# Optimization experiments

Hardware: AMD Instinct MI355X
Metric: run time of the kernel (lower is better)

The kernel has to match this reference:

```python
import jax, jax.numpy as jnp
import numpy as np

N = 50000
E = 800000
IN_DIM = 128
HIDDEN = 256
HEADS = 8
HEAD_DIM = HIDDEN // HEADS  # 32
NUM_CLASSES = 40
NEG_SLOPE = 0.2


def setup_inputs() -> dict:
    key = jax.random.key(0)
    ks = jax.random.split(key, 16)
    x = jax.random.normal(ks[0], (N, IN_DIM), dtype=jnp.float32)
    edge_index = jax.random.randint(ks[1], (2, E), 0, N, dtype=jnp.int64)

    def glorot(k, shape, fan_in):
        return jax.random.normal(k, shape, dtype=jnp.float32) / np.sqrt(fan_in)

    # layer 1: in -> heads*head_dim (concat)
    W1 = glorot(ks[2], (IN_DIM, HEADS * HEAD_DIM), IN_DIM)
    as1 = glorot(ks[3], (HEADS, HEAD_DIM), HEAD_DIM)
    ad1 = glorot(ks[4], (HEADS, HEAD_DIM), HEAD_DIM)
    b1 = jnp.zeros((HEADS * HEAD_DIM,), dtype=jnp.float32)
    # layer 2: hidden -> heads*head_dim (concat)
    W2 = glorot(ks[5], (HIDDEN, HEADS * HEAD_DIM), HIDDEN)
    as2 = glorot(ks[6], (HEADS, HEAD_DIM), HEAD_DIM)
    ad2 = glorot(ks[7], (HEADS, HEAD_DIM), HEAD_DIM)
    b2 = jnp.zeros((HEADS * HEAD_DIM,), dtype=jnp.float32)
    # layer 3: hidden -> num_classes, 1 head, no concat (mean == identity for 1 head)
    W3 = glorot(ks[8], (HIDDEN, 1 * NUM_CLASSES), HIDDEN)
    as3 = glorot(ks[9], (1, NUM_CLASSES), NUM_CLASSES)
    ad3 = glorot(ks[10], (1, NUM_CLASSES), NUM_CLASSES)
    b3 = jnp.zeros((NUM_CLASSES,), dtype=jnp.float32)
    return {"x": x, "edge_index": edge_index,
            "W1": W1, "as1": as1, "ad1": ad1, "b1": b1,
            "W2": W2, "as2": as2, "ad2": ad2, "b2": b2,
            "W3": W3, "as3": as3, "ad3": ad3, "b3": b3}


def _segment_softmax(logits, seg, n):
    # logits: [E, H]; softmax per destination node
    m = jax.ops.segment_max(logits, seg, num_segments=n)
    m = jnp.where(jnp.isfinite(m), m, 0.0)  # empty segments -> 0
    e = jnp.exp(logits - m[seg])
    s = jax.ops.segment_sum(e, seg, num_segments=n)
    return e / (s[seg] + 1e-16)


def _gat_layer(x, src, dst, W, a_src, a_dst, b, heads, concat):
    n = x.shape[0]
    h = (x @ W).reshape(n, heads, -1)                    # [N, H, D]
    al_s = jnp.einsum('nhd,hd->nh', h, a_src)            # [N, H]
    al_d = jnp.einsum('nhd,hd->nh', h, a_dst)            # [N, H]
    e = jax.nn.leaky_relu(al_s[src] + al_d[dst], NEG_SLOPE)  # [E, H]
    alpha = _segment_softmax(e, dst, n)                  # [E, H]
    msg = h[src] * alpha[..., None]                      # [E, H, D]
    out = jax.ops.segment_sum(msg, dst, num_segments=n)  # [N, H, D]
    out = out.reshape(n, -1) if concat else out.mean(axis=1)
    return out + b


def reference(x, edge_index, W1, as1, ad1, b1, W2, as2, ad2, b2, W3, as3, ad3, b3):
    # add self loops (PyG GATConv default)
    loops = jnp.arange(N, dtype=edge_index.dtype)
    src = jnp.concatenate([edge_index[0], loops])
    dst = jnp.concatenate([edge_index[1], loops])
    # eval mode: dropout is a no-op
    h = _gat_layer(x, src, dst, W1, as1, ad1, b1, HEADS, True)
    h = jax.nn.elu(h)
    h = _gat_layer(h, src, dst, W2, as2, ad2, b2, HEADS, True)
    h = jax.nn.elu(h)
    out = _gat_layer(h, src, dst, W3, as3, ad3, b3, 1, False)
    return out
```

## Files before the change

kernel.cpp:

```cpp
#include <hip/hip_runtime.h>
#include <hip/hip_bf16.h>

#define NEG_SLOPE 0.2f

typedef __attribute__((ext_vector_type(8))) short bf16x8;
typedef __attribute__((ext_vector_type(4))) float f32x4;

__device__ __forceinline__ unsigned short f2bf(float v) {
    union { float f; unsigned int u; } x; x.f = v;
    unsigned int r = x.u + 0x7fffu + ((x.u >> 16) & 1u);
    return (unsigned short)(r >> 16);
}
__device__ __forceinline__ float bf2f(unsigned short b) {
    union { unsigned int u; float f; } x; x.u = ((unsigned int)b) << 16;
    return x.f;
}


__global__ void count_edges_k(const int* __restrict__ ei, int E, int n, int* __restrict__ cnt) {
    int e = blockIdx.x * 256 + threadIdx.x;
    int ET = E + n;
    if (e >= ET) return;
    int d = (e < E) ? ei[E + e] : (e - E);
    atomicAdd(&cnt[d], 1);
}

__global__ void scan1_k(const int* __restrict__ cnt, int* __restrict__ row_ptr,
                        int* __restrict__ bsums, int n) {
    __shared__ int sd[256];
    int b = blockIdx.x, t = threadIdx.x;
    int base = b * 1024 + t * 4;
    int v[4];
    int loc = 0;
#pragma unroll
    for (int j = 0; j < 4; ++j) {
        v[j] = (base + j < n) ? cnt[base + j] : 0;
        loc += v[j];
    }
    sd[t] = loc;
    __syncthreads();
    for (int off = 1; off < 256; off <<= 1) {
        int x = (t >= off) ? sd[t - off] : 0;
        __syncthreads();
        sd[t] += x;
        __syncthreads();
    }
    int run = sd[t] - loc;
    if (t == 255) bsums[b] = sd[t];
#pragma unroll
    for (int j = 0; j < 4; ++j) {
        if (base + j < n) row_ptr[base + j] = run;
        run += v[j];
    }
}

__global__ void scan2_k(int* __restrict__ bsums, int nb) {
    if (threadIdx.x == 0 && blockIdx.x == 0) {
        int run = 0;
        for (int i = 0; i < nb; ++i) { int x = bsums[i]; bsums[i] = run; run += x; }
    }
}

__global__ void scan3_k(int* __restrict__ row_ptr, int* __restrict__ pos,
                        const int* __restrict__ bsums, int n, int total) {
    int idx = blockIdx.x * 256 + threadIdx.x;
    if (idx < n) {
        int vv = row_ptr[idx] + bsums[idx >> 10];
        row_ptr[idx] = vv;
        pos[idx] = vv;
    } else if (idx == n) {
        row_ptr[n] = total;
    }
}

__global__ void scatter_edges_k(const int* __restrict__ ei, int E, int n,
                                int* __restrict__ pos, int* __restrict__ srcs) {
    int e = blockIdx.x * 256 + threadIdx.x;
    int ET = E + n;
    if (e >= ET) return;
    int s, d;
    if (e < E) { s = ei[e]; d = ei[E + e]; }
    else       { s = e - E; d = e - E; }
    int idx = atomicAdd(&pos[d], 1);
    srcs[idx] = s;
}


__global__ void convert_w_k(const float* __restrict__ W,
                            unsigned short* __restrict__ Bh, unsigned short* __restrict__ Bl,
                            int K, int Nc) {
    int idx = blockIdx.x * 256 + threadIdx.x;
    if (idx >= K * Nc) return;
    int k = idx / Nc, c = idx - k * Nc;
    float v = W[idx];
    unsigned short h = f2bf(v);
    float r = v - bf2f(h);
    Bh[c * K + k] = h;
    Bl[c * K + k] = f2bf(r);
}


#define GPAD 40

__global__ __launch_bounds__(256) void mfma_gemm_k(const float* __restrict__ A,
                                                   const unsigned short* __restrict__ Bh,
                                                   const unsigned short* __restrict__ Bl,
                                                   unsigned short* __restrict__ Cb,
                                                   int M, int K, int Nc) {
    __shared__ unsigned short Ash[128][GPAD];
    __shared__ unsigned short Asl[128][GPAD];
    __shared__ unsigned short Bsh[128][GPAD];
    __shared__ unsigned short Bsl[128][GPAD];

    int bm = blockIdx.y * 128;
    int bn = blockIdx.x * 128;
    int t = threadIdx.x;
    int w = t >> 6, l = t & 63;
    int wm = w >> 1, wn = w & 1;
    int lr = l & 15, lk = (l >> 4) * 8;

    int srow = t >> 1;
    int skh  = (t & 1) * 16;

    f32x4 acc[4][4];
#pragma unroll
    for (int i = 0; i < 4; ++i)
#pragma unroll
        for (int j = 0; j < 4; ++j)
            acc[i][j] = (f32x4){0.f, 0.f, 0.f, 0.f};

    const int arow = bm + srow;
    const bool arow_ok = (arow < M);
    const size_t acol_base = (size_t)arow * K + skh;
    const size_t bcol_base = (size_t)(bn + srow) * K + skh;

    for (int k0 = 0; k0 < K; k0 += 32) {
        float vv[16];
        if (arow_ok) {
            const float4* ap = reinterpret_cast<const float4*>(A + acol_base + k0);
#pragma unroll
            for (int q = 0; q < 4; ++q) {
                float4 v4 = ap[q];
                vv[4 * q + 0] = v4.x; vv[4 * q + 1] = v4.y;
                vv[4 * q + 2] = v4.z; vv[4 * q + 3] = v4.w;
            }
        } else {
#pragma unroll
            for (int q = 0; q < 16; ++q) vv[q] = 0.f;
        }
        unsigned int hw[8], lw[8];
#pragma unroll
        for (int q = 0; q < 8; ++q) {
            unsigned short h0 = f2bf(vv[2 * q]);
            unsigned short h1 = f2bf(vv[2 * q + 1]);
            unsigned short l0 = f2bf(vv[2 * q] - bf2f(h0));
            unsigned short l1 = f2bf(vv[2 * q + 1] - bf2f(h1));
            hw[q] = (unsigned int)h0 | ((unsigned int)h1 << 16);
            lw[q] = (unsigned int)l0 | ((unsigned int)l1 << 16);
        }
        __syncthreads();
        {
            uint4* dh = reinterpret_cast<uint4*>(&Ash[srow][skh]);
            uint4* dl = reinterpret_cast<uint4*>(&Asl[srow][skh]);
            dh[0] = make_uint4(hw[0], hw[1], hw[2], hw[3]);
            dh[1] = make_uint4(hw[4], hw[5], hw[6], hw[7]);
            dl[0] = make_uint4(lw[0], lw[1], lw[2], lw[3]);
            dl[1] = make_uint4(lw[4], lw[5], lw[6], lw[7]);
        }
        {
            const uint4* sh = reinterpret_cast<const uint4*>(Bh + bcol_base + k0);
            const uint4* sl = reinterpret_cast<const uint4*>(Bl + bcol_base + k0);
            uint4* dh = reinterpret_cast<uint4*>(&Bsh[srow][skh]);
            uint4* dl = reinterpret_cast<uint4*>(&Bsl[srow][skh]);
            dh[0] = sh[0]; dh[1] = sh[1];
            dl[0] = sl[0]; dl[1] = sl[1];
        }
        __syncthreads();

        bf16x8 ah[4], al[4], bh[4], bl[4];
#pragma unroll
        for (int i = 0; i < 4; ++i) {
            int r = wm * 64 + i * 16 + lr;
            ah[i] = *reinterpret_cast<const bf16x8*>(&Ash[r][lk]);
            al[i] = *reinterpret_cast<const bf16x8*>(&Asl[r][lk]);
        }
#pragma unroll
        for (int j = 0; j < 4; ++j) {
            int c = wn * 64 + j * 16 + lr;
            bh[j] = *reinterpret_cast<const bf16x8*>(&Bsh[c][lk]);
            bl[j] = *reinterpret_cast<const bf16x8*>(&Bsl[c][lk]);
        }
#pragma unroll
        for (int i = 0; i < 4; ++i)
#pragma unroll
            for (int j = 0; j < 4; ++j) {
                acc[i][j] = __builtin_amdgcn_mfma_f32_16x16x32_bf16(ah[i], bh[j], acc[i][j], 0, 0, 0);
                acc[i][j] = __builtin_amdgcn_mfma_f32_16x16x32_bf16(ah[i], bl[j], acc[i][j], 0, 0, 0);
                acc[i][j] = __builtin_amdgcn_mfma_f32_16x16x32_bf16(al[i], bh[j], acc[i][j], 0, 0, 0);
            }
    }

#pragma unroll
    for (int i = 0; i < 4; ++i) {
#pragma unroll
        for (int r = 0; r < 4; ++r) {
            int row_g = bm + wm * 64 + i * 16 + (l >> 4) * 4 + r;
            if (row_g >= M) continue;
#pragma unroll
            for (int j = 0; j < 4; ++j) {
                int col_g = bn + wn * 64 + j * 16 + lr;
                Cb[(size_t)row_g * Nc + col_g] = f2bf(acc[i][j][r]);
            }
        }
    }
}


__global__ __launch_bounds__(256) void gemm_bf16a_k(const unsigned short* __restrict__ A,
                                                    const unsigned short* __restrict__ Bh,
                                                    const unsigned short* __restrict__ Bl,
                                                    unsigned short* __restrict__ Cb,
                                                    int M, int K, int Nc) {
    __shared__ unsigned short As[128][GPAD];
    __shared__ unsigned short Bsh[128][GPAD];
    __shared__ unsigned short Bsl[128][GPAD];

    int bm = blockIdx.y * 128;
    int bn = blockIdx.x * 128;
    int t = threadIdx.x;
    int w = t >> 6, l = t & 63;
    int wm = w >> 1, wn = w & 1;
    int lr = l & 15, lk = (l >> 4) * 8;

    int srow = t >> 1;
    int skh  = (t & 1) * 16;

    f32x4 acc[4][4];
#pragma unroll
    for (int i = 0; i < 4; ++i)
#pragma unroll
        for (int j = 0; j < 4; ++j)
            acc[i][j] = (f32x4){0.f, 0.f, 0.f, 0.f};

    const int arow = bm + srow;
    const bool arow_ok = (arow < M);
    const size_t acol_base = (size_t)arow * K + skh;
    const size_t bcol_base = (size_t)(bn + srow) * K + skh;

    for (int k0 = 0; k0 < K; k0 += 32) {
        __syncthreads();
        {
            uint4* da = reinterpret_cast<uint4*>(&As[srow][skh]);
            if (arow_ok) {
                const uint4* sa = reinterpret_cast<const uint4*>(A + acol_base + k0);
                da[0] = sa[0]; da[1] = sa[1];
            } else {
                da[0] = make_uint4(0u, 0u, 0u, 0u);
                da[1] = make_uint4(0u, 0u, 0u, 0u);
            }
            const uint4* sh = reinterpret_cast<const uint4*>(Bh + bcol_base + k0);
            const uint4* sl = reinterpret_cast<const uint4*>(Bl + bcol_base + k0);
            uint4* dh = reinterpret_cast<uint4*>(&Bsh[srow][skh]);
            uint4* dl = reinterpret_cast<uint4*>(&Bsl[srow][skh]);
            dh[0] = sh[0]; dh[1] = sh[1];
            dl[0] = sl[0]; dl[1] = sl[1];
        }
        __syncthreads();

        bf16x8 ah[4], bh[4], bl[4];
#pragma unroll
        for (int i = 0; i < 4; ++i) {
            int r = wm * 64 + i * 16 + lr;
            ah[i] = *reinterpret_cast<const bf16x8*>(&As[r][lk]);
        }
#pragma unroll
        for (int j = 0; j < 4; ++j) {
            int c = wn * 64 + j * 16 + lr;
            bh[j] = *reinterpret_cast<const bf16x8*>(&Bsh[c][lk]);
            bl[j] = *reinterpret_cast<const bf16x8*>(&Bsl[c][lk]);
        }
#pragma unroll
        for (int i = 0; i < 4; ++i)
#pragma unroll
            for (int j = 0; j < 4; ++j) {
                acc[i][j] = __builtin_amdgcn_mfma_f32_16x16x32_bf16(ah[i], bh[j], acc[i][j], 0, 0, 0);
                acc[i][j] = __builtin_amdgcn_mfma_f32_16x16x32_bf16(ah[i], bl[j], acc[i][j], 0, 0, 0);
            }
    }

#pragma unroll
    for (int i = 0; i < 4; ++i) {
#pragma unroll
        for (int r = 0; r < 4; ++r) {
            int row_g = bm + wm * 64 + i * 16 + (l >> 4) * 4 + r;
            if (row_g >= M) continue;
#pragma unroll
            for (int j = 0; j < 4; ++j) {
                int col_g = bn + wn * 64 + j * 16 + lr;
                Cb[(size_t)row_g * Nc + col_g] = f2bf(acc[i][j][r]);
            }
        }
    }
}


__global__ __launch_bounds__(256) void compute_al_k(const unsigned short* __restrict__ h,
                                                    const float* __restrict__ a_src,
                                                    const float* __restrict__ a_dst,
                                                    float* __restrict__ al_s,
                                                    float* __restrict__ al_d, int n) {
    int wid = threadIdx.x >> 6, lane = threadIdx.x & 63;
    int node = blockIdx.x * 4 + wid;
    if (node >= n) return;
    ushort4 v = reinterpret_cast<const ushort4*>(h + (size_t)node * 256)[lane];
    float4 asv = reinterpret_cast<const float4*>(a_src)[lane];
    float4 adv = reinterpret_cast<const float4*>(a_dst)[lane];
    float ps = bf2f(v.x) * asv.x + bf2f(v.y) * asv.y + bf2f(v.z) * asv.z + bf2f(v.w) * asv.w;
    float pd = bf2f(v.x) * adv.x + bf2f(v.y) * adv.y + bf2f(v.z) * adv.z + bf2f(v.w) * adv.w;
#pragma unroll
    for (int off = 1; off < 8; off <<= 1) {
        ps += __shfl_xor(ps, off, 64);
        pd += __shfl_xor(pd, off, 64);
    }
    if ((lane & 7) == 0) {
        al_s[node * 8 + (lane >> 3)] = ps;
        al_d[node * 8 + (lane >> 3)] = pd;
    }
}

__global__ void compute_al3_k(const unsigned short* __restrict__ h,
                              const float* __restrict__ a_src, const float* __restrict__ a_dst,
                              float* __restrict__ al_s, float* __restrict__ al_d, int n) {
    int wid = threadIdx.x >> 6, lane = threadIdx.x & 63;
    int node = blockIdx.x * 4 + wid;
    if (node >= n) return;
    float hv = (lane < 40) ? bf2f(h[(size_t)node * 128 + lane]) : 0.f;
    float ps = (lane < 40) ? hv * a_src[lane] : 0.f;
    float pd = (lane < 40) ? hv * a_dst[lane] : 0.f;
#pragma unroll
    for (int off = 32; off; off >>= 1) {
        ps += __shfl_xor(ps, off, 64);
        pd += __shfl_xor(pd, off, 64);
    }
    if (lane == 0) { al_s[node] = ps; al_d[node] = pd; }
}


__global__ __launch_bounds__(256) void edge_softmax_k(const float* __restrict__ al_s,
                                                      const float* __restrict__ al_d,
                                                      const int* __restrict__ row_ptr,
                                                      const int* __restrict__ srcs,
                                                      float* __restrict__ w,
                                                      float* __restrict__ inv, int n8) {
    int tid = blockIdx.x * 256 + threadIdx.x;
    if (tid >= n8) return;
    int dst = tid >> 3, hd = tid & 7;
    int beg = row_ptr[dst], end = row_ptr[dst + 1];
    float ald = al_d[tid];

    float m = -1e30f;
    int i = beg;
    for (; i + 2 <= end; i += 2) {
        int s0 = srcs[i], s1 = srcs[i + 1];
        float l0 = al_s[s0 * 8 + hd] + ald;
        float l1 = al_s[s1 * 8 + hd] + ald;
        l0 = (l0 > 0.f) ? l0 : NEG_SLOPE * l0;
        l1 = (l1 > 0.f) ? l1 : NEG_SLOPE * l1;
        m = fmaxf(m, fmaxf(l0, l1));
    }
    if (i < end) {
        int s0 = srcs[i];
        float l0 = al_s[s0 * 8 + hd] + ald;
        l0 = (l0 > 0.f) ? l0 : NEG_SLOPE * l0;
        m = fmaxf(m, l0);
    }

    float sw = 0.f;
    for (i = beg; i < end; ++i) {
        int s = srcs[i];
        float l = al_s[s * 8 + hd] + ald;
        l = (l > 0.f) ? l : NEG_SLOPE * l;
        float e = __expf(l - m);
        w[(size_t)i * 8 + hd] = e;
        sw += e;
    }
    inv[tid] = 1.f / (sw + 1e-16f);
}

__global__ __launch_bounds__(256) void edge_softmax3_k(const float* __restrict__ al_s,
                                                       const float* __restrict__ al_d,
                                                       const int* __restrict__ row_ptr,
                                                       const int* __restrict__ srcs,
                                                       float* __restrict__ w,
                                                       float* __restrict__ inv, int n) {
    int dst = blockIdx.x * 256 + threadIdx.x;
    if (dst >= n) return;
    int beg = row_ptr[dst], end = row_ptr[dst + 1];
    float ald = al_d[dst];

    float m = -1e30f;
    int i = beg;
    for (; i + 2 <= end; i += 2) {
        int s0 = srcs[i], s1 = srcs[i + 1];
        float l0 = al_s[s0] + ald;
        float l1 = al_s[s1] + ald;
        l0 = (l0 > 0.f) ? l0 : NEG_SLOPE * l0;
        l1 = (l1 > 0.f) ? l1 : NEG_SLOPE * l1;
        m = fmaxf(m, fmaxf(l0, l1));
    }
    if (i < end) {
        int s0 = srcs[i];
        float l0 = al_s[s0] + ald;
        l0 = (l0 > 0.f) ? l0 : NEG_SLOPE * l0;
        m = fmaxf(m, l0);
    }

    float sw = 0.f;
    for (i = beg; i < end; ++i) {
        int s = srcs[i];
        float l = al_s[s] + ald;
        l = (l > 0.f) ? l : NEG_SLOPE * l;
        float e = __expf(l - m);
        w[i] = e;
        sw += e;
    }
    inv[dst] = 1.f / (sw + 1e-16f);
}


template <bool ELU>
__global__ __launch_bounds__(256) void gat_gather_k(const unsigned short* __restrict__ h,
                                                    const float* __restrict__ w,
                                                    const float* __restrict__ inv,
                                                    const int* __restrict__ row_ptr,
                                                    const int* __restrict__ srcs,
                                                    const float* __restrict__ bias,
                                                    unsigned short* __restrict__ out, int n) {
    int wid = threadIdx.x >> 6, lane = threadIdx.x & 63;
    int dst = blockIdx.x * 4 + wid;
    if (dst >= n) return;
    int hd = lane >> 3;
    int beg = row_ptr[dst], end = row_ptr[dst + 1];
    const ushort4* hp = reinterpret_cast<const ushort4*>(h);

    float4 acc = make_float4(0.f, 0.f, 0.f, 0.f);
    int i = beg;
    for (; i + 4 <= end; i += 4) {
        int s0 = srcs[i + 0], s1 = srcs[i + 1], s2 = srcs[i + 2], s3 = srcs[i + 3];
        float w0 = w[(size_t)(i + 0) * 8 + hd];
        float w1 = w[(size_t)(i + 1) * 8 + hd];
        float w2 = w[(size_t)(i + 2) * 8 + hd];
        float w3 = w[(size_t)(i + 3) * 8 + hd];
        ushort4 v0 = hp[(size_t)s0 * 64 + lane];
        ushort4 v1 = hp[(size_t)s1 * 64 + lane];
        ushort4 v2 = hp[(size_t)s2 * 64 + lane];
        ushort4 v3 = hp[(size_t)s3 * 64 + lane];
        acc.x = fmaf(w0, bf2f(v0.x), acc.x);
        acc.y = fmaf(w0, bf2f(v0.y), acc.y);
        acc.z = fmaf(w0, bf2f(v0.z), acc.z);
        acc.w = fmaf(w0, bf2f(v0.w), acc.w);
        acc.x = fmaf(w1, bf2f(v1.x), acc.x);
        acc.y = fmaf(w1, bf2f(v1.y), acc.y);
        acc.z = fmaf(w1, bf2f(v1.z), acc.z);
        acc.w = fmaf(w1, bf2f(v1.w), acc.w);
        acc.x = fmaf(w2, bf2f(v2.x), acc.x);
        acc.y = fmaf(w2, bf2f(v2.y), acc.y);
        acc.z = fmaf(w2, bf2f(v2.z), acc.z);
        acc.w = fmaf(w2, bf2f(v2.w), acc.w);
        acc.x = fmaf(w3, bf2f(v3.x), acc.x);
        acc.y = fmaf(w3, bf2f(v3.y), acc.y);
        acc.z = fmaf(w3, bf2f(v3.z), acc.z);
        acc.w = fmaf(w3, bf2f(v3.w), acc.w);
    }
    for (; i < end; ++i) {
        int s = srcs[i];
        float wgt = w[(size_t)i * 8 + hd];
        ushort4 v = hp[(size_t)s * 64 + lane];
        acc.x = fmaf(wgt, bf2f(v.x), acc.x);
        acc.y = fmaf(wgt, bf2f(v.y), acc.y);
        acc.z = fmaf(wgt, bf2f(v.z), acc.z);
        acc.w = fmaf(wgt, bf2f(v.w), acc.w);
    }

    float iv = inv[dst * 8 + hd];
    float4 b4 = reinterpret_cast<const float4*>(bias)[lane];
    float4 o;
    o.x = acc.x * iv + b4.x;
    o.y = acc.y * iv + b4.y;
    o.z = acc.z * iv + b4.z;
    o.w = acc.w * iv + b4.w;
    if (ELU) {
        o.x = (o.x > 0.f) ? o.x : expm1f(o.x);
        o.y = (o.y > 0.f) ? o.y : expm1f(o.y);
        o.z = (o.z > 0.f) ? o.z : expm1f(o.z);
        o.w = (o.w > 0.f) ? o.w : expm1f(o.w);
    }
    ushort4 ob;
    ob.x = f2bf(o.x); ob.y = f2bf(o.y); ob.z = f2bf(o.z); ob.w = f2bf(o.w);
    reinterpret_cast<ushort4*>(out + (size_t)dst * 256)[lane] = ob;
}

__global__ __launch_bounds__(256) void gat_gather3_k(const unsigned short* __restrict__ h,
                                                     const float* __restrict__ w,
                                                     const float* __restrict__ inv,
                                                     const int* __restrict__ row_ptr,
                                                     const int* __restrict__ srcs,
                                                     const float* __restrict__ bias,
                                                     float* __restrict__ out, int n) {
    int wid = threadIdx.x >> 6, lane = threadIdx.x & 63;
    int dst = blockIdx.x * 4 + wid;
    if (dst >= n) return;
    int es = lane >> 4, cl = lane & 15;
    int beg = row_ptr[dst], end = row_ptr[dst + 1];

    float4 acc = make_float4(0.f, 0.f, 0.f, 0.f);
    for (int i = beg; i < end; i += 4) {
        int idx = i + es;
        bool ok = (idx < end);
        int s = ok ? srcs[idx] : srcs[beg];
        float wgt = ok ? w[idx] : 0.f;
        ushort4 v = reinterpret_cast<const ushort4*>(h + (size_t)s * 128)[cl];
        acc.x = fmaf(wgt, bf2f(v.x), acc.x);
        acc.y = fmaf(wgt, bf2f(v.y), acc.y);
        acc.z = fmaf(wgt, bf2f(v.z), acc.z);
        acc.w = fmaf(wgt, bf2f(v.w), acc.w);
    }
#pragma unroll
    for (int off = 16; off <= 32; off <<= 1) {
        acc.x += __shfl_xor(acc.x, off, 64);
        acc.y += __shfl_xor(acc.y, off, 64);
        acc.z += __shfl_xor(acc.z, off, 64);
        acc.w += __shfl_xor(acc.w, off, 64);
    }
    if (es == 0 && cl < 10) {
        float iv = inv[dst];
        int c = cl * 4;
        float4 b4 = *reinterpret_cast<const float4*>(bias + c);
        float4 o;
        o.x = acc.x * iv + b4.x;
        o.y = acc.y * iv + b4.y;
        o.z = acc.z * iv + b4.z;
        o.w = acc.w * iv + b4.w;
        *reinterpret_cast<float4*>(out + (size_t)dst * 40 + c) = o;
    }
}


extern "C" void kernel_launch(void* const* d_in, const int* in_sizes, int n_in,
                              void* d_out, int out_size, void* d_ws, size_t ws_size,
                              hipStream_t stream) {
    const float* x   = (const float*)d_in[0];
    const int*   ei  = (const int*)d_in[1];
    const float* W1  = (const float*)d_in[2];
    const float* as1 = (const float*)d_in[3];
    const float* ad1 = (const float*)d_in[4];
    const float* b1  = (const float*)d_in[5];
    const float* W2  = (const float*)d_in[6];
    const float* as2 = (const float*)d_in[7];
    const float* ad2 = (const float*)d_in[8];
    const float* b2  = (const float*)d_in[9];
    const float* W3  = (const float*)d_in[10];
    const float* as3 = (const float*)d_in[11];
    const float* ad3 = (const float*)d_in[12];
    const float* b3  = (const float*)d_in[13];

    const int N = in_sizes[0] / 128;
    const int E = in_sizes[1] / 2;
    const int ET = E + N;

    char* ws = (char*)d_ws;
    size_t off = 0;
    auto alloc = [&](size_t bytes) -> void* {
        void* p = ws + off;
        off += (bytes + 255) & ~(size_t)255;
        return p;
    };
    int*   row_ptr = (int*)alloc(sizeof(int) * (N + 1));
    int*   pos     = (int*)alloc(sizeof(int) * N);
    int*   srcs    = (int*)alloc(sizeof(int) * ET);
    int*   bsums   = (int*)alloc(sizeof(int) * 64);
    float* als     = (float*)alloc(sizeof(float) * N * 8);
    float* ald     = (float*)alloc(sizeof(float) * N * 8);
    float* wbuf    = (float*)alloc(sizeof(float) * (size_t)ET * 8);
    float* invb    = (float*)alloc(sizeof(float) * N * 8);
    unsigned short* hb16 = (unsigned short*)alloc(sizeof(unsigned short) * (size_t)N * 256);
    unsigned short* ab16 = (unsigned short*)alloc(sizeof(unsigned short) * (size_t)N * 256);
    unsigned short* wbh  = (unsigned short*)alloc(sizeof(unsigned short) * 256 * 256);
    unsigned short* wbl  = (unsigned short*)alloc(sizeof(unsigned short) * 256 * 256);
    (void)ws_size;

    const int nb = (N + 1023) / 1024;

    hipMemsetAsync(pos, 0, sizeof(int) * N, stream);
    count_edges_k<<<(ET + 255) / 256, 256, 0, stream>>>(ei, E, N, pos);
    scan1_k<<<nb, 256, 0, stream>>>(pos, row_ptr, bsums, N);
    scan2_k<<<1, 64, 0, stream>>>(bsums, nb);
    scan3_k<<<(N + 1 + 255) / 256, 256, 0, stream>>>(row_ptr, pos, bsums, N, ET);
    scatter_edges_k<<<(ET + 255) / 256, 256, 0, stream>>>(ei, E, N, pos, srcs);

    const int gy = (N + 127) / 128;
    const int gagg = (N + 3) / 4;
    const int gsm = (N * 8 + 255) / 256;

    convert_w_k<<<(128 * 256 + 255) / 256, 256, 0, stream>>>(W1, wbh, wbl, 128, 256);
    mfma_gemm_k<<<dim3(2, gy), 256, 0, stream>>>(x, wbh, wbl, hb16, N, 128, 256);
    compute_al_k<<<gagg, 256, 0, stream>>>(hb16, as1, ad1, als, ald, N);
    edge_softmax_k<<<gsm, 256, 0, stream>>>(als, ald, row_ptr, srcs, wbuf, invb, N * 8);
    gat_gather_k<true><<<gagg, 256, 0, stream>>>(hb16, wbuf, invb, row_ptr, srcs, b1, ab16, N);

    convert_w_k<<<(256 * 256 + 255) / 256, 256, 0, stream>>>(W2, wbh, wbl, 256, 256);
    gemm_bf16a_k<<<dim3(2, gy), 256, 0, stream>>>(ab16, wbh, wbl, hb16, N, 256, 256);
    compute_al_k<<<gagg, 256, 0, stream>>>(hb16, as2, ad2, als, ald, N);
    edge_softmax_k<<<gsm, 256, 0, stream>>>(als, ald, row_ptr, srcs, wbuf, invb, N * 8);
    gat_gather_k<true><<<gagg, 256, 0, stream>>>(hb16, wbuf, invb, row_ptr, srcs, b2, ab16, N);

    hipMemsetAsync(wbh, 0, sizeof(unsigned short) * 128 * 256, stream);
    hipMemsetAsync(wbl, 0, sizeof(unsigned short) * 128 * 256, stream);
    convert_w_k<<<(256 * 40 + 255) / 256, 256, 0, stream>>>(W3, wbh, wbl, 256, 40);
    gemm_bf16a_k<<<dim3(1, gy), 256, 0, stream>>>(ab16, wbh, wbl, hb16, N, 256, 128);
    compute_al3_k<<<gagg, 256, 0, stream>>>(hb16, as3, ad3, als, ald, N);
    edge_softmax3_k<<<(N + 255) / 256, 256, 0, stream>>>(als, ald, row_ptr, srcs, wbuf, invb, N);
    gat_gather3_k<<<gagg, 256, 0, stream>>>(hb16, wbuf, invb, row_ptr, srcs, b3, (float*)d_out, N);
}
```

Measured before the change: 444.1 us.

## Merge weight conversions into one kernel and use grid-stride gather loops

Folds the three per-layer weight conversion launches and the two memsets into a single kernel at the start, with separate buffers for each layer (W3 padded to 128 columns inside the kernel). The gather and attention-logit kernels switch to a fixed grid of 2048 blocks with grid-stride loops over nodes instead of one wave per node. The softmax exp pass is unrolled by two. This removes launch and memset overhead and amortises per-wave setup, but fewer resident waves may hide less gather latency.

```diff
diff --git a/kernel.cpp b/kernel.cpp
--- a/kernel.cpp
+++ b/kernel.cpp
@@ -86,17 +86,38 @@
 }
 
 
-__global__ void convert_w_k(const float* __restrict__ W,
-                            unsigned short* __restrict__ Bh, unsigned short* __restrict__ Bl,
-                            int K, int Nc) {
+#define R1 (128 * 256)
+#define R2 (256 * 256)
+#define R3 (256 * 128)
+
+__global__ void convert_w_all_k(const float* __restrict__ W1, const float* __restrict__ W2,
+                                const float* __restrict__ W3,
+                                unsigned short* __restrict__ b1h, unsigned short* __restrict__ b1l,
+                                unsigned short* __restrict__ b2h, unsigned short* __restrict__ b2l,
+                                unsigned short* __restrict__ b3h, unsigned short* __restrict__ b3l) {
     int idx = blockIdx.x * 256 + threadIdx.x;
-    if (idx >= K * Nc) return;
-    int k = idx / Nc, c = idx - k * Nc;
-    float v = W[idx];
+    float v;
+    unsigned short* dh;
+    unsigned short* dl;
+    int o;
+    if (idx < R1) {
+        int k = idx >> 8, c = idx & 255;
+        v = W1[idx]; dh = b1h; dl = b1l; o = c * 128 + k;
+    } else if (idx < R1 + R2) {
+        int j = idx - R1;
+        int k = j >> 8, c = j & 255;
+        v = W2[j]; dh = b2h; dl = b2l; o = c * 256 + k;
+    } else if (idx < R1 + R2 + R3) {
+        int j = idx - (R1 + R2);
+        int k = j >> 7, c = j & 127;
+        v = (c < 40) ? W3[k * 40 + c] : 0.f;
+        dh = b3h; dl = b3l; o = c * 256 + k;
+    } else {
+        return;
+    }
     unsigned short h = f2bf(v);
-    float r = v - bf2f(h);
-    Bh[c * K + k] = h;
-    Bl[c * K + k] = f2bf(r);
+    dh[o] = h;
+    dl[o] = f2bf(v - bf2f(h));
 }
 
 
@@ -309,22 +330,24 @@
                                                     const float* __restrict__ a_dst,
                                                     float* __restrict__ al_s,
                                                     float* __restrict__ al_d, int n) {
-    int wid = threadIdx.x >> 6, lane = threadIdx.x & 63;
-    int node = blockIdx.x * 4 + wid;
-    if (node >= n) return;
-    ushort4 v = reinterpret_cast<const ushort4*>(h + (size_t)node * 256)[lane];
+    int gw = blockIdx.x * 4 + (threadIdx.x >> 6);
+    int nw = gridDim.x * 4;
+    int lane = threadIdx.x & 63;
     float4 asv = reinterpret_cast<const float4*>(a_src)[lane];
     float4 adv = reinterpret_cast<const float4*>(a_dst)[lane];
-    float ps = bf2f(v.x) * asv.x + bf2f(v.y) * asv.y + bf2f(v.z) * asv.z + bf2f(v.w) * asv.w;
-    float pd = bf2f(v.x) * adv.x + bf2f(v.y) * adv.y + bf2f(v.z) * adv.z + bf2f(v.w) * adv.w;
-#pragma unroll
-    for (int off = 1; off < 8; off <<= 1) {
-        ps += __shfl_xor(ps, off, 64);
-        pd += __shfl_xor(pd, off, 64);
-    }
-    if ((lane & 7) == 0) {
-        al_s[node * 8 + (lane >> 3)] = ps;
-        al_d[node * 8 + (lane >> 3)] = pd;
+    for (int node = gw; node < n; node += nw) {
+        ushort4 v = reinterpret_cast<const ushort4*>(h + (size_t)node * 256)[lane];
+        float ps = bf2f(v.x) * asv.x + bf2f(v.y) * asv.y + bf2f(v.z) * asv.z + bf2f(v.w) * asv.w;
+        float pd = bf2f(v.x) * adv.x + bf2f(v.y) * adv.y + bf2f(v.z) * adv.z + bf2f(v.w) * adv.w;
+#pragma unroll
+        for (int off = 1; off < 8; off <<= 1) {
+            ps += __shfl_xor(ps, off, 64);
+            pd += __shfl_xor(pd, off, 64);
+        }
+        if ((lane & 7) == 0) {
+            al_s[node * 8 + (lane >> 3)] = ps;
+            al_d[node * 8 + (lane >> 3)] = pd;
+        }
     }
 }
 
@@ -376,7 +399,20 @@
     }
 
     float sw = 0.f;
-    for (i = beg; i < end; ++i) {
+    i = beg;
+    for (; i + 2 <= end; i += 2) {
+        int s0 = srcs[i], s1 = srcs[i + 1];
+        float l0 = al_s[s0 * 8 + hd] + ald;
+        float l1 = al_s[s1 * 8 + hd] + ald;
+        l0 = (l0 > 0.f) ? l0 : NEG_SLOPE * l0;
+        l1 = (l1 > 0.f) ? l1 : NEG_SLOPE * l1;
+        float e0 = __expf(l0 - m);
+        float e1 = __expf(l1 - m);
+        w[(size_t)i * 8 + hd] = e0;
+        w[(size_t)(i + 1) * 8 + hd] = e1;
+        sw += e0 + e1;
+    }
+    if (i < end) {
         int s = srcs[i];
         float l = al_s[s * 8 + hd] + ald;
         l = (l > 0.f) ? l : NEG_SLOPE * l;
@@ -436,68 +472,70 @@
                                                     const int* __restrict__ srcs,
                                                     const float* __restrict__ bias,
                                                     unsigned short* __restrict__ out, int n) {
-    int wid = threadIdx.x >> 6, lane = threadIdx.x & 63;
-    int dst = blockIdx.x * 4 + wid;
-    if (dst >= n) return;
+    int gw = blockIdx.x * 4 + (threadIdx.x >> 6);
+    int nw = gridDim.x * 4;
+    int lane = threadIdx.x & 63;
     int hd = lane >> 3;
-    int beg = row_ptr[dst], end = row_ptr[dst + 1];
     const ushort4* hp = reinterpret_cast<const ushort4*>(h);
-
-    float4 acc = make_float4(0.f, 0.f, 0.f, 0.f);
-    int i = beg;
-    for (; i + 4 <= end; i += 4) {
-        int s0 = srcs[i + 0], s1 = srcs[i + 1], s2 = srcs[i + 2], s3 = srcs[i + 3];
-        float w0 = w[(size_t)(i + 0) * 8 + hd];
-        float w1 = w[(size_t)(i + 1) * 8 + hd];
-        float w2 = w[(size_t)(i + 2) * 8 + hd];
-        float w3 = w[(size_t)(i + 3) * 8 + hd];
-        ushort4 v0 = hp[(size_t)s0 * 64 + lane];
-        ushort4 v1 = hp[(size_t)s1 * 64 + lane];
-        ushort4 v2 = hp[(size_t)s2 * 64 + lane];
-        ushort4 v3 = hp[(size_t)s3 * 64 + lane];
-        acc.x = fmaf(w0, bf2f(v0.x), acc.x);
-        acc.y = fmaf(w0, bf2f(v0.y), acc.y);
-        acc.z = fmaf(w0, bf2f(v0.z), acc.z);
-        acc.w = fmaf(w0, bf2f(v0.w), acc.w);
-        acc.x = fmaf(w1, bf2f(v1.x), acc.x);
-        acc.y = fmaf(w1, bf2f(v1.y), acc.y);
-        acc.z = fmaf(w1, bf2f(v1.z), acc.z);
-        acc.w = fmaf(w1, bf2f(v1.w), acc.w);
-        acc.x = fmaf(w2, bf2f(v2.x), acc.x);
-        acc.y = fmaf(w2, bf2f(v2.y), acc.y);
-        acc.z = fmaf(w2, bf2f(v2.z), acc.z);
-        acc.w = fmaf(w2, bf2f(v2.w), acc.w);
-        acc.x = fmaf(w3, bf2f(v3.x), acc.x);
-        acc.y = fmaf(w3, bf2f(v3.y), acc.y);
-        acc.z = fmaf(w3, bf2f(v3.z), acc.z);
-        acc.w = fmaf(w3, bf2f(v3.w), acc.w);
-    }
-    for (; i < end; ++i) {
-        int s = srcs[i];
-        float wgt = w[(size_t)i * 8 + hd];
-        ushort4 v = hp[(size_t)s * 64 + lane];
-        acc.x = fmaf(wgt, bf2f(v.x), acc.x);
-        acc.y = fmaf(wgt, bf2f(v.y), acc.y);
-        acc.z = fmaf(wgt, bf2f(v.z), acc.z);
-        acc.w = fmaf(wgt, bf2f(v.w), acc.w);
-    }
-
-    float iv = inv[dst * 8 + hd];
     float4 b4 = reinterpret_cast<const float4*>(bias)[lane];
-    float4 o;
-    o.x = acc.x * iv + b4.x;
-    o.y = acc.y * iv + b4.y;
-    o.z = acc.z * iv + b4.z;
-    o.w = acc.w * iv + b4.w;
-    if (ELU) {
-        o.x = (o.x > 0.f) ? o.x : expm1f(o.x);
-        o.y = (o.y > 0.f) ? o.y : expm1f(o.y);
-        o.z = (o.z > 0.f) ? o.z : expm1f(o.z);
-        o.w = (o.w > 0.f) ? o.w : expm1f(o.w);
-    }
-    ushort4 ob;
-    ob.x = f2bf(o.x); ob.y = f2bf(o.y); ob.z = f2bf(o.z); ob.w = f2bf(o.w);
-    reinterpret_cast<ushort4*>(out + (size_t)dst * 256)[lane] = ob;
+
+    for (int dst = gw; dst < n; dst += nw) {
+        int beg = row_ptr[dst], end = row_ptr[dst + 1];
+        float4 acc = make_float4(0.f, 0.f, 0.f, 0.f);
+        int i = beg;
+        for (; i + 4 <= end; i += 4) {
+            int s0 = srcs[i + 0], s1 = srcs[i + 1], s2 = srcs[i + 2], s3 = srcs[i + 3];
+            float w0 = w[(size_t)(i + 0) * 8 + hd];
+            float w1 = w[(size_t)(i + 1) * 8 + hd];
+            float w2 = w[(size_t)(i + 2) * 8 + hd];
+            float w3 = w[(size_t)(i + 3) * 8 + hd];
+            ushort4 v0 = hp[(size_t)s0 * 64 + lane];
+            ushort4 v1 = hp[(size_t)s1 * 64 + lane];
+            ushort4 v2 = hp[(size_t)s2 * 64 + lane];
+            ushort4 v3 = hp[(size_t)s3 * 64 + lane];
+            acc.x = fmaf(w0, bf2f(v0.x), acc.x);
+            acc.y = fmaf(w0, bf2f(v0.y), acc.y);
+            acc.z = fmaf(w0, bf2f(v0.z), acc.z);
+            acc.w = fmaf(w0, bf2f(v0.w), acc.w);
+            acc.x = fmaf(w1, bf2f(v1.x), acc.x);
+            acc.y = fmaf(w1, bf2f(v1.y), acc.y);
+            acc.z = fmaf(w1, bf2f(v1.z), acc.z);
+            acc.w = fmaf(w1, bf2f(v1.w), acc.w);
+            acc.x = fmaf(w2, bf2f(v2.x), acc.x);
+            acc.y = fmaf(w2, bf2f(v2.y), acc.y);
+            acc.z = fmaf(w2, bf2f(v2.z), acc.z);
+            acc.w = fmaf(w2, bf2f(v2.w), acc.w);
+            acc.x = fmaf(w3, bf2f(v3.x), acc.x);
+            acc.y = fmaf(w3, bf2f(v3.y), acc.y);
+            acc.z = fmaf(w3, bf2f(v3.z), acc.z);
+            acc.w = fmaf(w3, bf2f(v3.w), acc.w);
+        }
+        for (; i < end; ++i) {
+            int s = srcs[i];
+            float wgt = w[(size_t)i * 8 + hd];
+            ushort4 v = hp[(size_t)s * 64 + lane];
+            acc.x = fmaf(wgt, bf2f(v.x), acc.x);
+            acc.y = fmaf(wgt, bf2f(v.y), acc.y);
+            acc.z = fmaf(wgt, bf2f(v.z), acc.z);
+            acc.w = fmaf(wgt, bf2f(v.w), acc.w);
+        }
+
+        float iv = inv[dst * 8 + hd];
+        float4 o;
+        o.x = acc.x * iv + b4.x;
+        o.y = acc.y * iv + b4.y;
+        o.z = acc.z * iv + b4.z;
+        o.w = acc.w * iv + b4.w;
+        if (ELU) {
+            o.x = (o.x > 0.f) ? o.x : expm1f(o.x);
+            o.y = (o.y > 0.f) ? o.y : expm1f(o.y);
+            o.z = (o.z > 0.f) ? o.z : expm1f(o.z);
+            o.w = (o.w > 0.f) ? o.w : expm1f(o.w);
+        }
+        ushort4 ob;
+        ob.x = f2bf(o.x); ob.y = f2bf(o.y); ob.z = f2bf(o.z); ob.w = f2bf(o.w);
+        reinterpret_cast<ushort4*>(out + (size_t)dst * 256)[lane] = ob;
+    }
 }
 
 __global__ __launch_bounds__(256) void gat_gather3_k(const unsigned short* __restrict__ h,
@@ -507,41 +545,43 @@
                                                      const int* __restrict__ srcs,
                                                      const float* __restrict__ bias,
                                                      float* __restrict__ out, int n) {
-    int wid = threadIdx.x >> 6, lane = threadIdx.x & 63;
-    int dst = blockIdx.x * 4 + wid;
-    if (dst >= n) return;
+    int gw = blockIdx.x * 4 + (threadIdx.x >> 6);
+    int nw = gridDim.x * 4;
+    int lane = threadIdx.x & 63;
     int es = lane >> 4, cl = lane & 15;
-    int beg = row_ptr[dst], end = row_ptr[dst + 1];
-
-    float4 acc = make_float4(0.f, 0.f, 0.f, 0.f);
-    for (int i = beg; i < end; i += 4) {
-        int idx = i + es;
-        bool ok = (idx < end);
-        int s = ok ? srcs[idx] : srcs[beg];
-        float wgt = ok ? w[idx] : 0.f;
-        ushort4 v = reinterpret_cast<const ushort4*>(h + (size_t)s * 128)[cl];
-        acc.x = fmaf(wgt, bf2f(v.x), acc.x);
-        acc.y = fmaf(wgt, bf2f(v.y), acc.y);
-        acc.z = fmaf(wgt, bf2f(v.z), acc.z);
-        acc.w = fmaf(wgt, bf2f(v.w), acc.w);
-    }
-#pragma unroll
-    for (int off = 16; off <= 32; off <<= 1) {
-        acc.x += __shfl_xor(acc.x, off, 64);
-        acc.y += __shfl_xor(acc.y, off, 64);
-        acc.z += __shfl_xor(acc.z, off, 64);
-        acc.w += __shfl_xor(acc.w, off, 64);
-    }
-    if (es == 0 && cl < 10) {
-        float iv = inv[dst];
-        int c = cl * 4;
-        float4 b4 = *reinterpret_cast<const float4*>(bias + c);
-        float4 o;
-        o.x = acc.x * iv + b4.x;
-        o.y = acc.y * iv + b4.y;
-        o.z = acc.z * iv + b4.z;
-        o.w = acc.w * iv + b4.w;
-        *reinterpret_cast<float4*>(out + (size_t)dst * 40 + c) = o;
+
+    for (int dst = gw; dst < n; dst += nw) {
+        int beg = row_ptr[dst], end = row_ptr[dst + 1];
+        float4 acc = make_float4(0.f, 0.f, 0.f, 0.f);
+        for (int i = beg; i < end; i += 4) {
+            int idx = i + es;
+            bool ok = (idx < end);
+            int s = ok ? srcs[idx] : srcs[beg];
+            float wgt = ok ? w[idx] : 0.f;
+            ushort4 v = reinterpret_cast<const ushort4*>(h + (size_t)s * 128)[cl];
+            acc.x = fmaf(wgt, bf2f(v.x), acc.x);
+            acc.y = fmaf(wgt, bf2f(v.y), acc.y);
+            acc.z = fmaf(wgt, bf2f(v.z), acc.z);
+            acc.w = fmaf(wgt, bf2f(v.w), acc.w);
+        }
+#pragma unroll
+        for (int off = 16; off <= 32; off <<= 1) {
+            acc.x += __shfl_xor(acc.x, off, 64);
+            acc.y += __shfl_xor(acc.y, off, 64);
+            acc.z += __shfl_xor(acc.z, off, 64);
+            acc.w += __shfl_xor(acc.w, off, 64);
+        }
+        if (es == 0 && cl < 10) {
+            float iv = inv[dst];
+            int c = cl * 4;
+            float4 b4 = *reinterpret_cast<const float4*>(bias + c);
+            float4 o;
+            o.x = acc.x * iv + b4.x;
+            o.y = acc.y * iv + b4.y;
+            o.z = acc.z * iv + b4.z;
+            o.w = acc.w * iv + b4.w;
+            *reinterpret_cast<float4*>(out + (size_t)dst * 40 + c) = o;
+        }
     }
 }
 
@@ -585,11 +625,19 @@
     float* invb    = (float*)alloc(sizeof(float) * N * 8);
     unsigned short* hb16 = (unsigned short*)alloc(sizeof(unsigned short) * (size_t)N * 256);
     unsigned short* ab16 = (unsigned short*)alloc(sizeof(unsigned short) * (size_t)N * 256);
-    unsigned short* wbh  = (unsigned short*)alloc(sizeof(unsigned short) * 256 * 256);
-    unsigned short* wbl  = (unsigned short*)alloc(sizeof(unsigned short) * 256 * 256);
+    unsigned short* wb1h = (unsigned short*)alloc(sizeof(unsigned short) * 128 * 256);
+    unsigned short* wb1l = (unsigned short*)alloc(sizeof(unsigned short) * 128 * 256);
+    unsigned short* wb2h = (unsigned short*)alloc(sizeof(unsigned short) * 256 * 256);
+    unsigned short* wb2l = (unsigned short*)alloc(sizeof(unsigned short) * 256 * 256);
+    unsigned short* wb3h = (unsigned short*)alloc(sizeof(unsigned short) * 128 * 256);
+    unsigned short* wb3l = (unsigned short*)alloc(sizeof(unsigned short) * 128 * 256);
     (void)ws_size;
 
     const int nb = (N + 1023) / 1024;
+    const int PG = 2048;
+
+    convert_w_all_k<<<(R1 + R2 + R3 + 255) / 256, 256, 0, stream>>>(
+        W1, W2, W3, wb1h, wb1l, wb2h, wb2l, wb3h, wb3l);
 
     hipMemsetAsync(pos, 0, sizeof(int) * N, stream);
     count_edges_k<<<(ET + 255) / 256, 256, 0, stream>>>(ei, E, N, pos);
@@ -602,23 +650,18 @@
     const int gagg = (N + 3) / 4;
     const int gsm = (N * 8 + 255) / 256;
 
-    convert_w_k<<<(128 * 256 + 255) / 256, 256, 0, stream>>>(W1, wbh, wbl, 128, 256);
-    mfma_gemm_k<<<dim3(2, gy), 256, 0, stream>>>(x, wbh, wbl, hb16, N, 128, 256);
-    compute_al_k<<<gagg, 256, 0, stream>>>(hb16, as1, ad1, als, ald, N);
+    mfma_gemm_k<<<dim3(2, gy), 256, 0, stream>>>(x, wb1h, wb1l, hb16, N, 128, 256);
+    compute_al_k<<<PG, 256, 0, stream>>>(hb16, as1, ad1, als, ald, N);
     edge_softmax_k<<<gsm, 256, 0, stream>>>(als, ald, row_ptr, srcs, wbuf, invb, N * 8);
-    gat_gather_k<true><<<gagg, 256, 0, stream>>>(hb16, wbuf, invb, row_ptr, srcs, b1, ab16, N);
-
-    convert_w_k<<<(256 * 256 + 255) / 256, 256, 0, stream>>>(W2, wbh, wbl, 256, 256);
-    gemm_bf16a_k<<<dim3(2, gy), 256, 0, stream>>>(ab16, wbh, wbl, hb16, N, 256, 256);
-    compute_al_k<<<gagg, 256, 0, stream>>>(hb16, as2, ad2, als, ald, N);
+    gat_gather_k<true><<<PG, 256, 0, stream>>>(hb16, wbuf, invb, row_ptr, srcs, b1, ab16, N);
+
+    gemm_bf16a_k<<<dim3(2, gy), 256, 0, stream>>>(ab16, wb2h, wb2l, hb16, N, 256, 256);
+    compute_al_k<<<PG, 256, 0, stream>>>(hb16, as2, ad2, als, ald, N);
     edge_softmax_k<<<gsm, 256, 0, stream>>>(als, ald, row_ptr, srcs, wbuf, invb, N * 8);
-    gat_gather_k<true><<<gagg, 256, 0, stream>>>(hb16, wbuf, invb, row_ptr, srcs, b2, ab16, N);
-
-    hipMemsetAsync(wbh, 0, sizeof(unsigned short) * 128 * 256, stream);
-    hipMemsetAsync(wbl, 0, sizeof(unsigned short) * 128 * 256, stream);
-    convert_w_k<<<(256 * 40 + 255) / 256, 256, 0, stream>>>(W3, wbh, wbl, 256, 40);
-    gemm_bf16a_k<<<dim3(1, gy), 256, 0, stream>>>(ab16, wbh, wbl, hb16, N, 256, 128);
+    gat_gather_k<true><<<PG, 256, 0, stream>>>(hb16, wbuf, invb, row_ptr, srcs, b2, ab16, N);
+
+    gemm_bf16a_k<<<dim3(1, gy), 256, 0, stream>>>(ab16, wb3h, wb3l, hb16, N, 256, 128);
     compute_al3_k<<<gagg, 256, 0, stream>>>(hb16, as3, ad3, als, ald, N);
     edge_softmax3_k<<<(N + 255) / 256, 256, 0, stream>>>(als, ald, row_ptr, srcs, wbuf, invb, N);
-    gat_gather3_k<<<gagg, 256, 0, stream>>>(hb16, wbuf, invb, row_ptr, srcs, b3, (float*)d_out, N);
-}
+    gat_gather3_k<<<PG, 256, 0, stream>>>(hb16, wbuf, invb, row_ptr, srcs, b3, (float*)d_out, N);
+}
```

Measured after the change: 427.6 us. 1.04x faster.
